# Optimization experiments

Hardware: AMD Instinct MI355X
Metric: run time of the kernel (lower is better)

Reference implementation:

```python
import jax, jax.numpy as jnp
import numpy as np

B = 256        # queries
N = 196608     # gallery rows (48 chunks of 4096)
D3 = 1536      # signature dim = 3 * embedding_dim
K = 32         # retrieval_k
CHUNK = 4096   # Gallery.retrieve default chunk_size


def setup_inputs() -> dict:
    key = jax.random.key(0)
    kq, kg, km = jax.random.split(key, 3)
    q = jax.random.normal(kq, (B, D3), dtype=jnp.float32)
    q = q / jnp.linalg.norm(q, axis=-1, keepdims=True)  # already L2-normalised per docstring
    g = jax.random.normal(kg, (N, D3), dtype=jnp.float32)
    g = g / jnp.linalg.norm(g, axis=-1, keepdims=True)
    exclude_mask = jax.random.randint(km, (B, N), 0, 2).astype(jnp.bool_)
    return {"query_signature": q, "gallery_sigs": g, "exclude_mask": exclude_mask, "k": K}


def reference(query_signature, gallery_sigs, exclude_mask, k):
    """Faithful JAX port of Gallery.retrieve: chunked sim matmul with a
    running (online) top-k merge, never materialising the full (B, N) score
    matrix as a single live buffer."""
    Bq = query_signature.shape[0]
    n_chunks = gallery_sigs.shape[0] // CHUNK
    g_chunks = gallery_sigs.reshape(n_chunks, CHUNK, gallery_sigs.shape[1])
    m_chunks = exclude_mask.reshape(Bq, n_chunks, CHUNK).transpose(1, 0, 2)  # (n_chunks, B, CHUNK)
    starts = (jnp.arange(n_chunks, dtype=jnp.int32) * CHUNK)

    init = (jnp.full((Bq, k), -jnp.inf, query_signature.dtype),
            jnp.full((Bq, k), -1, jnp.int32))

    def step(carry, xs):
        best_s, best_i = carry
        gc, mc, start = xs
        scores = query_signature @ gc.T                      # (B, CHUNK)
        scores = jnp.where(mc, -jnp.inf, scores)             # masked_fill
        comb_s = jnp.concatenate([best_s, scores], axis=1)   # (B, k+CHUNK)
        local_idx = jnp.broadcast_to(start + jnp.arange(CHUNK, dtype=jnp.int32)[None, :],
                                     scores.shape)
        comb_i = jnp.concatenate([best_i, local_idx], axis=1)
        top_s, top_pos = jax.lax.top_k(comb_s, k)
        top_i = jnp.take_along_axis(comb_i, top_pos, axis=1)
        return (top_s, top_i), None

    (best_s, best_i), _ = jax.lax.scan(step, init, (g_chunks, m_chunks, starts))
    return best_i, best_s
```

## Files before the change

### kernel.cpp

```cpp
#include <hip/hip_runtime.h>
#include <stdint.h>

#define BQ    256
#define NG    196608
#define D3    1536
#define KK    32
#define KBP   16
#define WB    512
#define RPB   384
#define NR    128
#define NSTEPS 3
#define BK    64
#define NKS   24
#define NCAND (WB*KBP)
#define C64   64

typedef short  s16x8 __attribute__((ext_vector_type(8)));
typedef float  f32x4 __attribute__((ext_vector_type(4)));

#define NEG_INF (-__builtin_inff())

__device__ __forceinline__ unsigned f2bf1(float x) {
    unsigned u = __builtin_bit_cast(unsigned, x);
    return (u + 0x7fffu + ((u >> 16) & 1u)) >> 16;
}
__device__ __forceinline__ unsigned pack2(float lo, float hi) {
    return (f2bf1(hi) << 16) | f2bf1(lo);
}

__device__ __forceinline__ void topkb_insert(float (&bs)[KBP], int (&bi)[KBP],
                                             float s, int idx) {
    float cs = s; int ci = idx;
#pragma unroll
    for (int m = 0; m < KBP; ++m) {
        const bool sw = cs > bs[m];
        const float ts = sw ? bs[m] : cs;
        const int   ti = sw ? bi[m] : ci;
        bs[m] = sw ? cs : bs[m];
        bi[m] = sw ? ci : bi[m];
        cs = ts; ci = ti;
    }
}
__device__ __forceinline__ void top8_insert(float (&bs)[8], int (&bi)[8],
                                            float s, int idx) {
    float cs = s; int ci = idx;
#pragma unroll
    for (int m = 0; m < 8; ++m) {
        const bool sw = cs > bs[m];
        const float ts = sw ? bs[m] : cs;
        const int   ti = sw ? bi[m] : ci;
        bs[m] = sw ? cs : bs[m];
        bi[m] = sw ? ci : bi[m];
        cs = ts; ci = ti;
    }
}

__global__ __launch_bounds__(256)
void cvt_q(const float* __restrict__ Q, unsigned short* __restrict__ Qbf) {
    const int i = (blockIdx.x * 256 + threadIdx.x) * 8;
    const float4 a = *(const float4*)(Q + i);
    const float4 b = *(const float4*)(Q + i + 4);
    uint4 v;
    v.x = pack2(a.x, a.y); v.y = pack2(a.z, a.w);
    v.z = pack2(b.x, b.y); v.w = pack2(b.z, b.w);
    *(uint4*)(Qbf + i) = v;
}

__global__ __launch_bounds__(256, 2)
void score_mfma(const unsigned short* __restrict__ Qbf, const float* __restrict__ G,
                const int* __restrict__ M,
                float* __restrict__ cand_s, int* __restrict__ cand_i) {
    __shared__ __align__(16) char lds[49152];
    const int blk = blockIdx.x, t = threadIdx.x;
    const int w = t >> 6, l = t & 63;
    const int l15 = l & 15, l4 = l >> 4;

    float bs[KBP]; int bi[KBP];
#pragma unroll
    for (int m = 0; m < KBP; ++m) { bs[m] = NEG_INF; bi[m] = -1; }

    const int grow_blk = blk * RPB;

    for (int ns = 0; ns < NSTEPS; ++ns) {
        const int grow0 = grow_blk + ns * NR;
        f32x4 acc[4][8];
#pragma unroll
        for (int qt = 0; qt < 4; ++qt)
#pragma unroll
            for (int rt = 0; rt < 8; ++rt) acc[qt][rt] = (f32x4)0.0f;

        for (int ks = 0; ks < NKS; ++ks) {
            const int k0 = ks * BK;
            __syncthreads();
            {
                const unsigned short* src = Qbf + (size_t)t * D3 + k0;
                const int rb = t * 128, rx = (t & 7) << 4;
#pragma unroll
                for (int c = 0; c < 8; ++c) {
                    const uint4 v = *(const uint4*)(src + c * 8);
                    *(uint4*)(lds + ((rb + c * 16) ^ rx)) = v;
                }
            }
            {
                const int r = t >> 1, h = t & 1;
                const float* src = G + (size_t)(grow0 + r) * D3 + k0 + h * 32;
                float4 f[8];
#pragma unroll
                for (int c = 0; c < 8; ++c) f[c] = *(const float4*)(src + c * 4);
                const int ro = r * 128 + h * 64, rx = (r & 7) << 4;
#pragma unroll
                for (int c2 = 0; c2 < 4; ++c2) {
                    uint4 v;
                    v.x = pack2(f[2 * c2].x, f[2 * c2].y);
                    v.y = pack2(f[2 * c2].z, f[2 * c2].w);
                    v.z = pack2(f[2 * c2 + 1].x, f[2 * c2 + 1].y);
                    v.w = pack2(f[2 * c2 + 1].z, f[2 * c2 + 1].w);
                    *(uint4*)(lds + 32768 + ((ro + c2 * 16) ^ rx)) = v;
                }
            }
            __syncthreads();
#pragma unroll
            for (int sk = 0; sk < 2; ++sk) {
                const int koff = sk * 64 + l4 * 16;
                s16x8 a[4];
#pragma unroll
                for (int qt = 0; qt < 4; ++qt) {
                    const int row = w * 64 + qt * 16 + l15;
                    a[qt] = *(const s16x8*)(lds + ((row * 128 + koff) ^ ((row & 7) << 4)));
                }
#pragma unroll
                for (int rt = 0; rt < 8; ++rt) {
                    const int row = rt * 16 + l15;
                    const s16x8 b = *(const s16x8*)(lds + 32768 +
                                     ((row * 128 + koff) ^ ((row & 7) << 4)));
#pragma unroll
                    for (int qt = 0; qt < 4; ++qt)
                        acc[qt][rt] = __builtin_amdgcn_mfma_f32_16x16x32_bf16(
                            a[qt], b, acc[qt][rt], 0, 0, 0);
                }
            }
        }
        __syncthreads();
        float* Slw = (float*)(lds + w * 8448);
        const int q = t;
        const int* mrow = M + (size_t)q * NG + grow0;
#pragma unroll
        for (int rs = 0; rs < 4; ++rs) {
#pragma unroll
            for (int qt = 0; qt < 4; ++qt)
#pragma unroll
                for (int r2 = 0; r2 < 2; ++r2)
#pragma unroll
                    for (int reg = 0; reg < 4; ++reg) {
                        const int qloc = qt * 16 + l4 * 4 + reg;
                        const int nloc = r2 * 16 + l15;
                        Slw[qloc * 33 + nloc] = acc[qt][rs * 2 + r2][reg];
                    }
            __asm__ volatile("s_waitcnt lgkmcnt(0)" ::: "memory");
            const int row0 = rs * 32;
            unsigned mv32 = 0;
#pragma unroll
            for (int c = 0; c < 8; ++c) {
                const int4 mm = *(const int4*)(mrow + row0 + c * 4);
                mv32 |= (mm.x ? 1u : 0u) << (c * 4);
                mv32 |= (mm.y ? 1u : 0u) << (c * 4 + 1);
                mv32 |= (mm.z ? 1u : 0u) << (c * 4 + 2);
                mv32 |= (mm.w ? 1u : 0u) << (c * 4 + 3);
            }
            const float* sp = Slw + l * 33;
            for (int j = 0; j < 32; ++j) {
                const float s = sp[j];
                if (s > bs[KBP - 1] && !((mv32 >> j) & 1u))
                    topkb_insert(bs, bi, s, grow0 + row0 + j);
            }
            __asm__ volatile("s_waitcnt lgkmcnt(0)" ::: "memory");
        }
    }
    float* os = cand_s + ((size_t)t * WB + blk) * KBP;
    int*   oi = cand_i + ((size_t)t * WB + blk) * KBP;
#pragma unroll
    for (int m = 0; m < KBP; ++m) { os[m] = bs[m]; oi[m] = bi[m]; }
}

__global__ __launch_bounds__(256)
void merge_rescore(const float* __restrict__ cand_s, const int* __restrict__ cand_i,
                   const float* __restrict__ Q, const float* __restrict__ G,
                   float* __restrict__ out) {
    __shared__ float Ls[2048];
    __shared__ int   Li[2048];
    __shared__ int   sel[C64];
    __shared__ float Fs[C64];
    const int q = blockIdx.x, t = threadIdx.x, l = t & 63, w = t >> 6;
    const float* cs = cand_s + (size_t)q * NCAND;
    const int*   ci = cand_i + (size_t)q * NCAND;

    float b8[8]; int i8[8];
#pragma unroll
    for (int m = 0; m < 8; ++m) { b8[m] = NEG_INF; i8[m] = -1; }
    for (int j = 0; j < NCAND / 256; ++j) {
        const float s = cs[t + 256 * j];
        if (s > b8[7]) top8_insert(b8, i8, s, ci[t + 256 * j]);
    }
#pragma unroll
    for (int m = 0; m < 8; ++m) { Ls[t * 8 + m] = b8[m]; Li[t * 8 + m] = i8[m]; }
    __syncthreads();

    for (int r = 0; r < C64; ++r) {
        if (t < 64) {
            float ms = NEG_INF; int mi = 0x7fffffff, mp = -1;
            for (int jj = 0; jj < 32; ++jj) {
                const float s = Ls[l + 64 * jj];
                const int  id = Li[l + 64 * jj];
                if (s > ms || (s == ms && id < mi)) { ms = s; mi = id; mp = l + 64 * jj; }
            }
#pragma unroll
            for (int off = 32; off >= 1; off >>= 1) {
                const float s2 = __shfl_xor(ms, off);
                const int   i2 = __shfl_xor(mi, off);
                const int   p2 = __shfl_xor(mp, off);
                if (s2 > ms || (s2 == ms && i2 < mi)) { ms = s2; mi = i2; mp = p2; }
            }
            if (l == 0) { sel[r] = mi; if (mp >= 0) Ls[mp] = NEG_INF; }
        }
        __syncthreads();
    }

    const float* qr = Q + (size_t)q * D3;
    for (int i = w; i < C64; i += 4) {
        const int idx = sel[i];
        float a = 0.0f;
        if (idx >= 0) {
            const float* gr = G + (size_t)idx * D3;
#pragma unroll
            for (int j = 0; j < 24; ++j)
                a = __builtin_fmaf(gr[l + 64 * j], qr[l + 64 * j], a);
        }
#pragma unroll
        for (int off = 32; off >= 1; off >>= 1) a += __shfl_xor(a, off);
        if (idx < 0) a = NEG_INF;
        if (l == 0) Fs[i] = a;
    }
    __syncthreads();

    if (t < 64) {
        float s = Fs[l]; const int id = sel[l];
        for (int r = 0; r < KK; ++r) {
            float ms = s; int mi = id;
#pragma unroll
            for (int off = 32; off >= 1; off >>= 1) {
                const float s2 = __shfl_xor(ms, off);
                const int   i2 = __shfl_xor(mi, off);
                if (s2 > ms || (s2 == ms && i2 < mi)) { ms = s2; mi = i2; }
            }
            if (l == 0) {
                out[(size_t)q * KK + r] = (float)mi;
                out[(size_t)BQ * KK + (size_t)q * KK + r] = ms;
            }
            if (s == ms && id == mi) s = NEG_INF;
        }
    }
}

extern "C" void kernel_launch(void* const* d_in, const int* in_sizes, int n_in,
                              void* d_out, int out_size, void* d_ws, size_t ws_size,
                              hipStream_t stream) {
    (void)in_sizes; (void)n_in; (void)out_size; (void)ws_size;
    const float* Q = (const float*)d_in[0];
    const float* G = (const float*)d_in[1];
    const int*   M = (const int*)d_in[2];

    unsigned short* Qbf = (unsigned short*)d_ws;
    float* cand_s = (float*)((char*)d_ws + (1u << 20));
    int*   cand_i = (int*)((char*)d_ws + (1u << 20) +
                           (size_t)BQ * WB * KBP * sizeof(float));
    float* out = (float*)d_out;

    hipLaunchKernelGGL(cvt_q, dim3(192), dim3(256), 0, stream, Q, Qbf);
    hipLaunchKernelGGL(score_mfma, dim3(WB), dim3(256), 0, stream, Qbf, G, M, cand_s, cand_i);
    hipLaunchKernelGGL(merge_rescore, dim3(BQ), dim3(256), 0, stream, cand_s, cand_i, Q, G, out);
}
```

Baseline: 956.9 us.

## Double-buffer gallery tiles, read Q directly, prepack mask bits, trim merge barriers

Prefetches the next gallery K-slice into registers while MFMAs run on the current LDS buffer, using two LDS buffers and one barrier per step. Query bf16 fragments are now loaded straight from global memory (L2-resident) instead of being staged through LDS each step. The int mask is packed into bitwords by a separate kernel so the scoring kernel reads one uint4 per step. The merge kernel's selection loop also drops its per-iteration block barrier. The costs are an extra kernel launch, an extra pass over the full mask, and more global traffic for Q.

```diff
diff --git a/kernel.cpp b/kernel.cpp
--- a/kernel.cpp
+++ b/kernel.cpp
@@ -12,6 +12,7 @@
 #define NSTEPS 3
 #define BK    64
 #define NKS   24
+#define MW    (NG/32)
 #define NCAND (WB*KBP)
 #define C64   64
 
@@ -19,6 +20,9 @@
 typedef float  f32x4 __attribute__((ext_vector_type(4)));
 
 #define NEG_INF (-__builtin_inff())
+
+#define BAR() do { __asm__ volatile("s_waitcnt lgkmcnt(0)" ::: "memory"); \
+                   __builtin_amdgcn_s_barrier(); } while (0)
 
 __device__ __forceinline__ unsigned f2bf1(float x) {
     unsigned u = __builtin_bit_cast(unsigned, x);
@@ -66,48 +70,100 @@
     *(uint4*)(Qbf + i) = v;
 }
 
+__global__ __launch_bounds__(256)
+void pack_mask(const int* __restrict__ M, unsigned* __restrict__ Mb) {
+    const int id = blockIdx.x * 256 + threadIdx.x;
+    const int* src = M + (size_t)id * 32;
+    unsigned wbits = 0;
+#pragma unroll
+    for (int c = 0; c < 8; ++c) {
+        const int4 m = *(const int4*)(src + c * 4);
+        wbits |= (m.x ? 1u : 0u) << (c * 4 + 0);
+        wbits |= (m.y ? 1u : 0u) << (c * 4 + 1);
+        wbits |= (m.z ? 1u : 0u) << (c * 4 + 2);
+        wbits |= (m.w ? 1u : 0u) << (c * 4 + 3);
+    }
+    Mb[id] = wbits;
+}
+
 __global__ __launch_bounds__(256, 2)
 void score_mfma(const unsigned short* __restrict__ Qbf, const float* __restrict__ G,
-                const int* __restrict__ M,
+                const unsigned* __restrict__ Mb,
                 float* __restrict__ cand_s, int* __restrict__ cand_i) {
-    __shared__ __align__(16) char lds[49152];
+    __shared__ __align__(16) char lds[33792];
     const int blk = blockIdx.x, t = threadIdx.x;
     const int w = t >> 6, l = t & 63;
     const int l15 = l & 15, l4 = l >> 4;
+    const int r_st = t >> 1, h_st = t & 1;
+    const int rx_st = (r_st & 7) << 4;
 
     float bs[KBP]; int bi[KBP];
 #pragma unroll
     for (int m = 0; m < KBP; ++m) { bs[m] = NEG_INF; bi[m] = -1; }
 
-    const int grow_blk = blk * RPB;
-
     for (int ns = 0; ns < NSTEPS; ++ns) {
-        const int grow0 = grow_blk + ns * NR;
+        const int grow0 = blk * RPB + ns * NR;
+        const float* gbase = G + (size_t)(grow0 + r_st) * D3 + h_st * 32;
+
+        float4 f[8];
+#pragma unroll
+        for (int c = 0; c < 8; ++c) f[c] = *(const float4*)(gbase + c * 4);
+        BAR();
+        {
+            const int ro = r_st * 128 + h_st * 64;
+#pragma unroll
+            for (int c2 = 0; c2 < 4; ++c2) {
+                uint4 v;
+                v.x = pack2(f[2 * c2].x, f[2 * c2].y);
+                v.y = pack2(f[2 * c2].z, f[2 * c2].w);
+                v.z = pack2(f[2 * c2 + 1].x, f[2 * c2 + 1].y);
+                v.w = pack2(f[2 * c2 + 1].z, f[2 * c2 + 1].w);
+                *(uint4*)(lds + ((ro + c2 * 16) ^ rx_st)) = v;
+            }
+        }
+
         f32x4 acc[4][8];
 #pragma unroll
         for (int qt = 0; qt < 4; ++qt)
 #pragma unroll
             for (int rt = 0; rt < 8; ++rt) acc[qt][rt] = (f32x4)0.0f;
 
+        int cur = 0;
         for (int ks = 0; ks < NKS; ++ks) {
             const int k0 = ks * BK;
-            __syncthreads();
-            {
-                const unsigned short* src = Qbf + (size_t)t * D3 + k0;
-                const int rb = t * 128, rx = (t & 7) << 4;
-#pragma unroll
-                for (int c = 0; c < 8; ++c) {
-                    const uint4 v = *(const uint4*)(src + c * 8);
-                    *(uint4*)(lds + ((rb + c * 16) ^ rx)) = v;
+            if (ks < NKS - 1) {
+                const float* src = gbase + (k0 + BK);
+#pragma unroll
+                for (int c = 0; c < 8; ++c) f[c] = *(const float4*)(src + c * 4);
+            }
+            BAR();
+            __builtin_amdgcn_s_setprio(1);
+            const char* bufb = lds + cur * 16384;
+#pragma unroll
+            for (int sk = 0; sk < 2; ++sk) {
+                const int koff = sk * 64 + l4 * 16;
+                s16x8 a[4];
+#pragma unroll
+                for (int qt = 0; qt < 4; ++qt) {
+                    const int row = w * 64 + qt * 16 + l15;
+                    a[qt] = *(const s16x8*)((const char*)Qbf + (size_t)row * 3072 +
+                                            k0 * 2 + koff);
                 }
-            }
-            {
-                const int r = t >> 1, h = t & 1;
-                const float* src = G + (size_t)(grow0 + r) * D3 + k0 + h * 32;
-                float4 f[8];
-#pragma unroll
-                for (int c = 0; c < 8; ++c) f[c] = *(const float4*)(src + c * 4);
-                const int ro = r * 128 + h * 64, rx = (r & 7) << 4;
+#pragma unroll
+                for (int rt = 0; rt < 8; ++rt) {
+                    const int row = rt * 16 + l15;
+                    const s16x8 b = *(const s16x8*)(bufb +
+                                     ((row * 128 + koff) ^ ((row & 7) << 4)));
+#pragma unroll
+                    for (int qt = 0; qt < 4; ++qt)
+                        acc[qt][rt] = __builtin_amdgcn_mfma_f32_16x16x32_bf16(
+                            a[qt], b, acc[qt][rt], 0, 0, 0);
+                }
+            }
+            __builtin_amdgcn_s_setprio(0);
+            if (ks < NKS - 1) {
+                char* ob = lds + (cur ^ 1) * 16384;
+                const int ro = r_st * 128 + h_st * 64;
 #pragma unroll
                 for (int c2 = 0; c2 < 4; ++c2) {
                     uint4 v;
@@ -115,35 +171,16 @@
                     v.y = pack2(f[2 * c2].z, f[2 * c2].w);
                     v.z = pack2(f[2 * c2 + 1].x, f[2 * c2 + 1].y);
                     v.w = pack2(f[2 * c2 + 1].z, f[2 * c2 + 1].w);
-                    *(uint4*)(lds + 32768 + ((ro + c2 * 16) ^ rx)) = v;
+                    *(uint4*)(ob + ((ro + c2 * 16) ^ rx_st)) = v;
                 }
-            }
-            __syncthreads();
-#pragma unroll
-            for (int sk = 0; sk < 2; ++sk) {
-                const int koff = sk * 64 + l4 * 16;
-                s16x8 a[4];
-#pragma unroll
-                for (int qt = 0; qt < 4; ++qt) {
-                    const int row = w * 64 + qt * 16 + l15;
-                    a[qt] = *(const s16x8*)(lds + ((row * 128 + koff) ^ ((row & 7) << 4)));
-                }
-#pragma unroll
-                for (int rt = 0; rt < 8; ++rt) {
-                    const int row = rt * 16 + l15;
-                    const s16x8 b = *(const s16x8*)(lds + 32768 +
-                                     ((row * 128 + koff) ^ ((row & 7) << 4)));
-#pragma unroll
-                    for (int qt = 0; qt < 4; ++qt)
-                        acc[qt][rt] = __builtin_amdgcn_mfma_f32_16x16x32_bf16(
-                            a[qt], b, acc[qt][rt], 0, 0, 0);
-                }
-            }
-        }
-        __syncthreads();
+                cur ^= 1;
+            }
+        }
+        BAR();
         float* Slw = (float*)(lds + w * 8448);
         const int q = t;
-        const int* mrow = M + (size_t)q * NG + grow0;
+        const uint4 mw4 = *(const uint4*)(Mb + (size_t)q * MW + blk * 12 + ns * 4);
+        const unsigned mv[4] = {mw4.x, mw4.y, mw4.z, mw4.w};
 #pragma unroll
         for (int rs = 0; rs < 4; ++rs) {
 #pragma unroll
@@ -157,20 +194,12 @@
                         Slw[qloc * 33 + nloc] = acc[qt][rs * 2 + r2][reg];
                     }
             __asm__ volatile("s_waitcnt lgkmcnt(0)" ::: "memory");
+            const unsigned m32 = mv[rs];
             const int row0 = rs * 32;
-            unsigned mv32 = 0;
-#pragma unroll
-            for (int c = 0; c < 8; ++c) {
-                const int4 mm = *(const int4*)(mrow + row0 + c * 4);
-                mv32 |= (mm.x ? 1u : 0u) << (c * 4);
-                mv32 |= (mm.y ? 1u : 0u) << (c * 4 + 1);
-                mv32 |= (mm.z ? 1u : 0u) << (c * 4 + 2);
-                mv32 |= (mm.w ? 1u : 0u) << (c * 4 + 3);
-            }
             const float* sp = Slw + l * 33;
             for (int j = 0; j < 32; ++j) {
                 const float s = sp[j];
-                if (s > bs[KBP - 1] && !((mv32 >> j) & 1u))
+                if (s > bs[KBP - 1] && !((m32 >> j) & 1u))
                     topkb_insert(bs, bi, s, grow0 + row0 + j);
             }
             __asm__ volatile("s_waitcnt lgkmcnt(0)" ::: "memory");
@@ -205,8 +234,8 @@
     for (int m = 0; m < 8; ++m) { Ls[t * 8 + m] = b8[m]; Li[t * 8 + m] = i8[m]; }
     __syncthreads();
 
-    for (int r = 0; r < C64; ++r) {
-        if (t < 64) {
+    if (t < 64) {
+        for (int r = 0; r < C64; ++r) {
             float ms = NEG_INF; int mi = 0x7fffffff, mp = -1;
             for (int jj = 0; jj < 32; ++jj) {
                 const float s = Ls[l + 64 * jj];
@@ -221,9 +250,10 @@
                 if (s2 > ms || (s2 == ms && i2 < mi)) { ms = s2; mi = i2; mp = p2; }
             }
             if (l == 0) { sel[r] = mi; if (mp >= 0) Ls[mp] = NEG_INF; }
-        }
-        __syncthreads();
-    }
+            __asm__ volatile("s_waitcnt lgkmcnt(0)" ::: "memory");
+        }
+    }
+    __syncthreads();
 
     const float* qr = Q + (size_t)q * D3;
     for (int i = w; i < C64; i += 4) {
@@ -270,12 +300,13 @@
     const int*   M = (const int*)d_in[2];
 
     unsigned short* Qbf = (unsigned short*)d_ws;
-    float* cand_s = (float*)((char*)d_ws + (1u << 20));
-    int*   cand_i = (int*)((char*)d_ws + (1u << 20) +
-                           (size_t)BQ * WB * KBP * sizeof(float));
+    unsigned* Mbits = (unsigned*)((char*)d_ws + (1u << 20));
+    float* cand_s = (float*)((char*)d_ws + (8u << 20));
+    int*   cand_i = (int*)((char*)d_ws + (16u << 20));
     float* out = (float*)d_out;
 
     hipLaunchKernelGGL(cvt_q, dim3(192), dim3(256), 0, stream, Q, Qbf);
-    hipLaunchKernelGGL(score_mfma, dim3(WB), dim3(256), 0, stream, Qbf, G, M, cand_s, cand_i);
+    hipLaunchKernelGGL(pack_mask, dim3(BQ * MW / 256), dim3(256), 0, stream, M, Mbits);
+    hipLaunchKernelGGL(score_mfma, dim3(WB), dim3(256), 0, stream, Qbf, G, Mbits, cand_s, cand_i);
     hipLaunchKernelGGL(merge_rescore, dim3(BQ), dim3(256), 0, stream, cand_s, cand_i, Q, G, out);
 }
```

After: 965.0 us. No clear change (+0.8%).
